# Optimization experiments

Hardware: AMD Instinct MI355X
Metric: run time of the kernel (lower is better)

## Reference

```python
import jax, jax.numpy as jnp
import numpy as np

MARGIN = 0.5  # init kwarg 'margin'
TWO_N, D = 8192, 256


def setup_inputs() -> dict:
    key = jax.random.key(0)
    k1, k2 = jax.random.split(key)
    embeddings = jax.random.normal(k1, (TWO_N, D), dtype=jnp.float32)
    neg_mask = jax.random.bernoulli(k2, 0.5, (TWO_N, TWO_N))  # bool [2N, 2N]
    return {"embeddings": embeddings, "neg_mask": neg_mask}


def _cdist(x, y):
    # Euclidean pairwise distances via the Gram trick (matches torch.cdist p=2)
    x2 = jnp.sum(x * x, axis=-1)[:, None]
    y2 = jnp.sum(y * y, axis=-1)[None, :]
    sq = jnp.maximum(x2 + y2 - 2.0 * (x @ y.T), 0.0)
    return jnp.sqrt(sq + 1e-12)


def reference(embeddings, neg_mask):
    two_n = embeddings.shape[0]
    n = two_n // 2
    d = _cdist(embeddings, embeddings)  # [2N, 2N]
    # masked sum of exp(margin - d) per anchor row (vectorizes the python loop)
    exp_neg = jnp.where(neg_mask, jnp.exp(MARGIN - d), 0.0)
    row_sums = exp_neg.sum(axis=1)  # [2N]
    idx = jnp.arange(n)
    ap = d[idx, idx + n]  # anchor-positive distances [N]
    j = jnp.log(row_sums[:n] + row_sums[n:]) + ap  # [N]
    # original skips NaN entries before the mean
    valid = ~jnp.isnan(j)
    r2 = jnp.where(valid, jnp.square(jnp.maximum(j, 0.0)), 0.0)
    cnt = jnp.maximum(valid.sum(), 1).astype(r2.dtype)
    loss = r2.sum() / cnt / 2.0
    return loss
```

## Files before the change

kernel.cpp:

```cpp
#include <hip/hip_runtime.h>
#include <hip/hip_bf16.h>
#include <stdint.h>

#define TWO_N  8192
#define NHALF  4096
#define DDIM   256
#define MARGIN 0.5f
#define NTRI   2080

static const size_t OFF_EMB  = 0;
static const size_t OFF_X2   = 4u * 1024 * 1024;
static const size_t OFF_AP   = OFF_X2 + (size_t)TWO_N * 4;
static const size_t OFF_FLAG = OFF_AP + (size_t)NHALF * 4;
static const size_t OFF_PART = OFF_FLAG + 256;
static const size_t OFF_RS   = OFF_PART + 64ull * TWO_N * 4;

typedef __attribute__((ext_vector_type(8))) short bf16x8;
typedef __attribute__((ext_vector_type(4))) float f32x4;

__device__ inline ushort f2bf(float f) {
  uint32_t u = __float_as_uint(f);
  uint32_t r = (u + 0x7FFFu + ((u >> 16) & 1u)) >> 16;
  return (ushort)r;
}
__device__ inline float bf2f(ushort h) { return __uint_as_float((uint32_t)h << 16); }

__device__ inline void gload_lds16(const void* g, void* l) {
  __builtin_amdgcn_global_load_lds(
      (const __attribute__((address_space(1))) uint32_t*)(uintptr_t)g,
      (__attribute__((address_space(3))) uint32_t*)(uint32_t)(uintptr_t)l,
      16, 0, 0);
}

#define STR2(x) #x
#define WAITVM(N) asm volatile("s_waitcnt vmcnt(" STR2(N) ")" ::: "memory")

__global__ __launch_bounds__(256) void smv2_prep(
    const float* __restrict__ emb,
    const uint32_t* __restrict__ maskw,
    ushort* __restrict__ emb_bf,
    float* __restrict__ x2,
    int* __restrict__ flag)
{
  const int t = threadIdx.x;
  if (blockIdx.x == 0) {
    __shared__ int sflag;
    if (t == 0) sflag = 0;
    __syncthreads();
    int found = 0;
    #pragma unroll
    for (int k = 0; k < 8; ++k) {
      uint32_t w = maskw[t * 8 + k];
      if (w > 1u && (w & 0xFEFEFEFEu) == 0u) found = 1;
    }
    if (found) atomicOr(&sflag, 1);
    __syncthreads();
    if (t == 0) *flag = sflag;
  }
  const int row  = blockIdx.x * 8 + (t >> 5);
  const int lane = t & 31;
  const float* rp = emb + (size_t)row * DDIM + lane * 8;
  float4 v0 = *(const float4*)(rp);
  float4 v1 = *(const float4*)(rp + 4);
  float vals[8] = {v0.x, v0.y, v0.z, v0.w, v1.x, v1.y, v1.z, v1.w};
  uint32_t packed[4];
  float ss = 0.f;
  #pragma unroll
  for (int k = 0; k < 4; ++k) {
    ushort h0 = f2bf(vals[2 * k]);
    ushort h1 = f2bf(vals[2 * k + 1]);
    packed[k] = (uint32_t)h0 | ((uint32_t)h1 << 16);
    float f0 = bf2f(h0), f1 = bf2f(h1);
    ss += f0 * f0 + f1 * f1;
  }
  *(uint4*)(emb_bf + (size_t)row * DDIM + lane * 8) =
      make_uint4(packed[0], packed[1], packed[2], packed[3]);
  #pragma unroll
  for (int m = 1; m < 32; m <<= 1) ss += __shfl_xor(ss, m);
  if (lane == 0) x2[row] = ss;
}

__global__ __launch_bounds__(512, 4) void smv2_main(
    const ushort* __restrict__ emb_bf,
    const float* __restrict__ x2,
    const uint8_t* __restrict__ mask8,
    const int* __restrict__ flagp,
    float* __restrict__ ap,
    float* __restrict__ partial)
{
  __shared__ char bufA[3 * 8192];
  __shared__ char bufB[3 * 8192];
  __shared__ uint8_t ldsM[128 * 128];
  __shared__ float ldsX[256];

  const int t = threadIdx.x;

  const int bid = blockIdx.x;
  const int idx = (bid & 7) * (NTRI / 8) + (bid >> 3);
  float rf = sqrtf(8.f * (float)idx + 1.f);
  int bx = (int)((rf - 1.f) * 0.5f);
  while ((bx + 1) * (bx + 2) / 2 <= idx) ++bx;
  while (bx * (bx + 1) / 2 > idx) --bx;
  const int by = idx - bx * (bx + 1) / 2;
  const int brow = by * 128;
  const int bcol = bx * 128;
  const bool diag = (bx == by);

  const char* gA = (const char*)(emb_bf + (size_t)brow * DDIM);
  const char* gB = (const char*)(emb_bf + (size_t)bcol * DDIM);

  const int srow = t >> 2;
  const int scb  = ((t & 3) * 16) ^ (((srow >> 1) & 3) << 4);
  const size_t gAoff = (size_t)srow * 512 + scb;
  const size_t gBoff = gAoff;
  const int ldst = t * 16;

  const int w  = t >> 6;
  const int l  = t & 63;
  const int wr = w >> 2;
  const int wc = w & 3;
  const int cl = l & 15;
  const int kh = l >> 4;

  int aoff[4], boff[2];
  #pragma unroll
  for (int m = 0; m < 4; ++m) {
    const int row = wr * 64 + m * 16 + cl;
    aoff[m] = row * 64 + ((kh * 16) ^ (((row >> 1) & 3) << 4));
  }
  #pragma unroll
  for (int n = 0; n < 2; ++n) {
    const int row = wc * 32 + n * 16 + cl;
    boff[n] = row * 64 + ((kh * 16) ^ (((row >> 1) & 3) << 4));
  }

  f32x4 acc[4][2];
  #pragma unroll
  for (int m = 0; m < 4; ++m)
    #pragma unroll
    for (int n = 0; n < 2; ++n) {
      f32x4 z = {0.f, 0.f, 0.f, 0.f};
      acc[m][n] = z;
    }
  uint32_t m2r[2][4];

#define STAGE(Q)                                                            \
  {                                                                         \
    gload_lds16(gA + gAoff + (Q) * 64, bufA + ((Q) % 3) * 8192 + ldst);     \
    gload_lds16(gB + gBoff + (Q) * 64, bufB + ((Q) % 3) * 8192 + ldst);     \
  }

#define M2LOAD                                                              \
  {                                                                         \
    _Pragma("unroll")                                                       \
    for (int n = 0; n < 2; ++n) {                                           \
      const int gj = bcol + wc * 32 + n * 16 + cl;                          \
      _Pragma("unroll")                                                     \
      for (int m = 0; m < 4; ++m)                                           \
        m2r[n][m] = *(const uint32_t*)(mask8 + (size_t)gj * TWO_N + brow +  \
                                       wr * 64 + m * 16 + kh * 4);          \
    }                                                                       \
  }

#define COMPUTE(P)                                                          \
  {                                                                         \
    const char* ba = bufA + ((P) % 3) * 8192;                               \
    const char* bb = bufB + ((P) % 3) * 8192;                               \
    bf16x8 a0 = *(const bf16x8*)(ba + aoff[0]);                             \
    bf16x8 a1 = *(const bf16x8*)(ba + aoff[1]);                             \
    bf16x8 a2 = *(const bf16x8*)(ba + aoff[2]);                             \
    bf16x8 a3 = *(const bf16x8*)(ba + aoff[3]);                             \
    bf16x8 b0 = *(const bf16x8*)(bb + boff[0]);                             \
    bf16x8 b1 = *(const bf16x8*)(bb + boff[1]);                             \
    acc[0][0] = __builtin_amdgcn_mfma_f32_16x16x32_bf16(a0, b0, acc[0][0], 0, 0, 0); \
    acc[0][1] = __builtin_amdgcn_mfma_f32_16x16x32_bf16(a0, b1, acc[0][1], 0, 0, 0); \
    acc[1][0] = __builtin_amdgcn_mfma_f32_16x16x32_bf16(a1, b0, acc[1][0], 0, 0, 0); \
    acc[1][1] = __builtin_amdgcn_mfma_f32_16x16x32_bf16(a1, b1, acc[1][1], 0, 0, 0); \
    acc[2][0] = __builtin_amdgcn_mfma_f32_16x16x32_bf16(a2, b0, acc[2][0], 0, 0, 0); \
    acc[2][1] = __builtin_amdgcn_mfma_f32_16x16x32_bf16(a2, b1, acc[2][1], 0, 0, 0); \
    acc[3][0] = __builtin_amdgcn_mfma_f32_16x16x32_bf16(a3, b0, acc[3][0], 0, 0, 0); \
    acc[3][1] = __builtin_amdgcn_mfma_f32_16x16x32_bf16(a3, b1, acc[3][1], 0, 0, 0); \
  }

#define PHASE(P, NW, SQ, DOM2)                                              \
  {                                                                         \
    WAITVM(NW);                                                             \
    __builtin_amdgcn_s_barrier();                                           \
    __builtin_amdgcn_sched_barrier(0);                                      \
    if ((SQ) >= 0) STAGE((SQ) < 0 ? 0 : (SQ));                              \
    if (DOM2) M2LOAD;                                                       \
    __builtin_amdgcn_sched_barrier(0);                                      \
    COMPUTE(P);                                                             \
  }

  STAGE(0);
  STAGE(1);
  #pragma unroll
  for (int it = 0; it < 2; ++it) {
    const int dl   = it * 8192 + t * 16;
    const int mrow = dl >> 7;
    const int mc   = dl & 127;
    const int msw  = ((mrow >> 2) & 3) << 5;
    gload_lds16(mask8 + (size_t)(brow + mrow) * TWO_N + bcol + (mc ^ msw), ldsM + dl);
  }
  {
    const float* src = (l < 32) ? (x2 + brow + l * 4) : (x2 + bcol + (l - 32) * 4);
    gload_lds16(src, (char*)ldsX + l * 16);
  }

  PHASE(0, 5, 2, 0)
  PHASE(1, 5, 3, 0)
  PHASE(2, 2, 4, 0)
  PHASE(3, 2, 5, 1)
  PHASE(4, 10, 6, 0)
  PHASE(5, 10, 7, 0)
  PHASE(6, 2, -1, 0)
  PHASE(7, 0, -1, 0)

  const int isByte = *flagp;
  const uint32_t* maskww = (const uint32_t*)mask8;

  float* part  = (float*)bufA;
  float* part2 = (float*)bufB;
  float cs[2] = {0.f, 0.f};

  #pragma unroll
  for (int m = 0; m < 4; ++m) {
    #pragma unroll
    for (int q = 0; q < 4; ++q) {
      const int lrow = wr * 64 + m * 16 + kh * 4 + q;
      const int gi = brow + lrow;
      const float xi = ldsX[lrow];
      const int msw = kh << 5;
      float rp = 0.f;
      #pragma unroll
      for (int n = 0; n < 2; ++n) {
        const int jc = wc * 32 + n * 16 + cl;
        const int gj = bcol + jc;
        const float g = acc[m][n][q];
        float sq = (gi == gj) ? 0.f : (xi + ldsX[128 + jc] - 2.f * g);
        sq = fmaxf(sq, 0.f) + 1e-12f;
        const float dd = __builtin_amdgcn_sqrtf(sq);
        if (gj == gi + NHALF && gi < NHALF) ap[gi] = dd;
        const float e = __expf(MARGIN - dd);
        bool mk1;
        if (isByte) mk1 = ldsM[lrow * 128 + (jc ^ msw)] != 0;
        else        mk1 = maskww[(size_t)gi * TWO_N + gj] != 0u;
        rp += mk1 ? e : 0.f;
        if (!diag) {
          bool mk2;
          if (isByte) mk2 = ((m2r[n][m] >> (8 * q)) & 255u) != 0u;
          else        mk2 = maskww[(size_t)gj * TWO_N + gi] != 0u;
          cs[n] += mk2 ? e : 0.f;
        }
      }
      #pragma unroll
      for (int s = 1; s < 16; s <<= 1) rp += __shfl_xor(rp, s);
      if (cl == 0) part[wc * 128 + lrow] = rp;
    }
  }

  if (!diag) {
    #pragma unroll
    for (int n = 0; n < 2; ++n) {
      cs[n] += __shfl_xor(cs[n], 16);
      cs[n] += __shfl_xor(cs[n], 32);
      if (l < 16) part2[wr * 128 + wc * 32 + n * 16 + l] = cs[n];
    }
  }
  __syncthreads();

  if (t < 128) {
    partial[(size_t)bx * TWO_N + brow + t] =
        (part[t] + part[128 + t]) + (part[256 + t] + part[384 + t]);
    if (!diag)
      partial[(size_t)by * TWO_N + bcol + t] = part2[t] + part2[128 + t];
  }
#undef PHASE
#undef COMPUTE
#undef M2LOAD
#undef STAGE
}

__global__ __launch_bounds__(256) void smv2_rowsum(
    const float* __restrict__ partial, float* __restrict__ rs)
{
  const int row = blockIdx.x * 256 + threadIdx.x;
  float s = 0.f;
  #pragma unroll 8
  for (int b = 0; b < 64; ++b) s += partial[(size_t)b * TWO_N + row];
  rs[row] = s;
}

__global__ __launch_bounds__(1024) void smv2_finalize(
    const float* __restrict__ rs, const float* __restrict__ ap,
    float* __restrict__ out)
{
  const int t = threadIdx.x;
  float sum = 0.f, cnt = 0.f;
  for (int i = t; i < NHALF; i += 1024) {
    float rsum = rs[i] + rs[i + NHALF];
    float jv = logf(rsum) + ap[i];
    if (!isnan(jv)) {
      cnt += 1.f;
      float mj = fmaxf(jv, 0.f);
      sum += mj * mj;
    }
  }
  __shared__ float ssum[16], scnt[16];
  #pragma unroll
  for (int s = 32; s >= 1; s >>= 1) {
    sum += __shfl_down(sum, s);
    cnt += __shfl_down(cnt, s);
  }
  const int wid = t >> 6, lid = t & 63;
  if (lid == 0) { ssum[wid] = sum; scnt[wid] = cnt; }
  __syncthreads();
  if (t == 0) {
    float S = 0.f, C = 0.f;
    #pragma unroll
    for (int i = 0; i < 16; ++i) { S += ssum[i]; C += scnt[i]; }
    if (C < 1.f) C = 1.f;
    out[0] = S / C * 0.5f;
  }
}

extern "C" void kernel_launch(void* const* d_in, const int* in_sizes, int n_in,
                              void* d_out, int out_size, void* d_ws, size_t ws_size,
                              hipStream_t stream) {
  const float* emb = (const float*)d_in[0];
  const void* mask = d_in[1];
  char* ws = (char*)d_ws;

  ushort* emb_bf = (ushort*)(ws + OFF_EMB);
  float*  x2     = (float*)(ws + OFF_X2);
  float*  ap     = (float*)(ws + OFF_AP);
  int*    flag   = (int*)(ws + OFF_FLAG);
  float*  part   = (float*)(ws + OFF_PART);
  float*  rs     = (float*)(ws + OFF_RS);

  smv2_prep<<<1024, 256, 0, stream>>>(emb, (const uint32_t*)mask, emb_bf, x2, flag);
  smv2_main<<<NTRI, 512, 0, stream>>>(emb_bf, x2, (const uint8_t*)mask, flag, ap, part);
  smv2_rowsum<<<32, 256, 0, stream>>>(part, rs);
  smv2_finalize<<<1, 1024, 0, stream>>>(rs, ap, (float*)d_out);
}
```

Baseline: 490.5 us.

## Pack mask into bitmap, simplify main pipeline, and accumulate row sums atomically

Adds a pack kernel that compresses the byte or word mask into a 1-bit-per-entry bitmap. The main kernel then reads small bitmap words for both the row and the transposed mask, instead of 16 KB byte tiles plus strided column loads. The main loop drops from triple to double buffering with plain barriers, and the occupancy hint rises to 8 blocks per CU. Per-tile partial row sums go to the result through atomics, which removes the separate row-sum kernel. In exchange it adds a full pass over the 64 MB mask, makes float accumulation order nondeterministic, and may leave the simpler pipeline less able to overlap loads with compute.

```diff
diff --git a/kernel.cpp b/kernel.cpp
--- a/kernel.cpp
+++ b/kernel.cpp
@@ -12,8 +12,8 @@
 static const size_t OFF_X2   = 4u * 1024 * 1024;
 static const size_t OFF_AP   = OFF_X2 + (size_t)TWO_N * 4;
 static const size_t OFF_FLAG = OFF_AP + (size_t)NHALF * 4;
-static const size_t OFF_PART = OFF_FLAG + 256;
-static const size_t OFF_RS   = OFF_PART + 64ull * TWO_N * 4;
+static const size_t OFF_BITM = 5u * 1024 * 1024;
+static const size_t OFF_RS   = 13u * 1024 * 1024;
 
 typedef __attribute__((ext_vector_type(8))) short bf16x8;
 typedef __attribute__((ext_vector_type(4))) float f32x4;
@@ -31,9 +31,12 @@
       (__attribute__((address_space(3))) uint32_t*)(uint32_t)(uintptr_t)l,
       16, 0, 0);
 }
-
-#define STR2(x) #x
-#define WAITVM(N) asm volatile("s_waitcnt vmcnt(" STR2(N) ")" ::: "memory")
+__device__ inline void gload_lds4(const void* g, void* l) {
+  __builtin_amdgcn_global_load_lds(
+      (const __attribute__((address_space(1))) uint32_t*)(uintptr_t)g,
+      (__attribute__((address_space(3))) uint32_t*)(uint32_t)(uintptr_t)l,
+      4, 0, 0);
+}
 
 __global__ __launch_bounds__(256) void smv2_prep(
     const float* __restrict__ emb,
@@ -80,17 +83,62 @@
   if (lane == 0) x2[row] = ss;
 }
 
-__global__ __launch_bounds__(512, 4) void smv2_main(
+__global__ __launch_bounds__(256) void smv2_pack(
+    const uint8_t* __restrict__ mask8,
+    const int* __restrict__ flagp,
+    uint32_t* __restrict__ bitM,
+    float* __restrict__ rs)
+{
+  const int t = threadIdx.x;
+  if (blockIdx.x == 0) {
+    float4 z = {0.f, 0.f, 0.f, 0.f};
+    #pragma unroll
+    for (int i = 0; i < 8; ++i) ((float4*)rs)[t * 8 + i] = z;
+  }
+  const int tid = blockIdx.x * 256 + t;
+  const int isByte = *flagp;
+  if (isByte) {
+    #pragma unroll
+    for (int it = 0; it < 4; ++it) {
+      const int idx = it * (2048 * 256) + tid;
+      const uint4 a = ((const uint4*)mask8)[(size_t)idx * 2];
+      const uint4 b = ((const uint4*)mask8)[(size_t)idx * 2 + 1];
+      const uint32_t wsv[8] = {a.x, a.y, a.z, a.w, b.x, b.y, b.z, b.w};
+      uint32_t out = 0;
+      #pragma unroll
+      for (int j = 0; j < 8; ++j)
+        out |= ((((wsv[j] & 0x01010101u) * 0x01020408u) >> 24) & 0xFu) << (4 * j);
+      bitM[idx] = out;
+    }
+  } else {
+    const uint32_t* maskw = (const uint32_t*)mask8;
+    #pragma unroll
+    for (int it = 0; it < 4; ++it) {
+      const int idx = it * (2048 * 256) + tid;
+      uint32_t out = 0;
+      #pragma unroll
+      for (int j = 0; j < 8; ++j) {
+        const uint4 wv = ((const uint4*)maskw)[(size_t)idx * 8 + j];
+        out |= (wv.x != 0u ? 1u : 0u) << (4 * j);
+        out |= (wv.y != 0u ? 1u : 0u) << (4 * j + 1);
+        out |= (wv.z != 0u ? 1u : 0u) << (4 * j + 2);
+        out |= (wv.w != 0u ? 1u : 0u) << (4 * j + 3);
+      }
+      bitM[idx] = out;
+    }
+  }
+}
+
+__global__ __launch_bounds__(512, 8) void smv2_main(
     const ushort* __restrict__ emb_bf,
     const float* __restrict__ x2,
-    const uint8_t* __restrict__ mask8,
-    const int* __restrict__ flagp,
+    const uint8_t* __restrict__ bitM,
     float* __restrict__ ap,
-    float* __restrict__ partial)
+    float* __restrict__ rs)
 {
-  __shared__ char bufA[3 * 8192];
-  __shared__ char bufB[3 * 8192];
-  __shared__ uint8_t ldsM[128 * 128];
+  __shared__ char bufA[2 * 8192];
+  __shared__ char bufB[2 * 8192];
+  __shared__ uint32_t ldsM[512];
   __shared__ float ldsX[256];
 
   const int t = threadIdx.x;
@@ -111,8 +159,7 @@
 
   const int srow = t >> 2;
   const int scb  = ((t & 3) * 16) ^ (((srow >> 1) & 3) << 4);
-  const size_t gAoff = (size_t)srow * 512 + scb;
-  const size_t gBoff = gAoff;
+  const size_t gOff = (size_t)srow * 512 + scb;
   const int ldst = t * 16;
 
   const int w  = t >> 6;
@@ -142,30 +189,36 @@
       f32x4 z = {0.f, 0.f, 0.f, 0.f};
       acc[m][n] = z;
     }
-  uint32_t m2r[2][4];
+
+  uint2 m2[2];
+  #pragma unroll
+  for (int n = 0; n < 2; ++n) {
+    const int gj = bcol + wc * 32 + n * 16 + cl;
+    m2[n] = *(const uint2*)(bitM + (size_t)gj * 1024 + (brow >> 3) + wr * 8);
+  }
+  __builtin_amdgcn_sched_barrier(0);
+
+  gload_lds4(bitM + (size_t)(brow + srow) * 1024 + (bcol >> 3) + (t & 3) * 4,
+             (char*)ldsM + t * 4);
+  {
+    const int xi = t & 255;
+    const float* src = (xi < 128) ? (x2 + brow + xi) : (x2 + bcol + (xi - 128));
+    gload_lds4(src, (char*)ldsX + xi * 4);
+  }
+  gload_lds16(gA + gOff, bufA + ldst);
+  gload_lds16(gB + gOff, bufB + ldst);
+  __syncthreads();
 
 #define STAGE(Q)                                                            \
   {                                                                         \
-    gload_lds16(gA + gAoff + (Q) * 64, bufA + ((Q) % 3) * 8192 + ldst);     \
-    gload_lds16(gB + gBoff + (Q) * 64, bufB + ((Q) % 3) * 8192 + ldst);     \
-  }
-
-#define M2LOAD                                                              \
-  {                                                                         \
-    _Pragma("unroll")                                                       \
-    for (int n = 0; n < 2; ++n) {                                           \
-      const int gj = bcol + wc * 32 + n * 16 + cl;                          \
-      _Pragma("unroll")                                                     \
-      for (int m = 0; m < 4; ++m)                                           \
-        m2r[n][m] = *(const uint32_t*)(mask8 + (size_t)gj * TWO_N + brow +  \
-                                       wr * 64 + m * 16 + kh * 4);          \
-    }                                                                       \
+    gload_lds16(gA + gOff + (Q) * 64, bufA + ((Q) & 1) * 8192 + ldst);      \
+    gload_lds16(gB + gOff + (Q) * 64, bufB + ((Q) & 1) * 8192 + ldst);      \
   }
 
 #define COMPUTE(P)                                                          \
   {                                                                         \
-    const char* ba = bufA + ((P) % 3) * 8192;                               \
-    const char* bb = bufB + ((P) % 3) * 8192;                               \
+    const char* ba = bufA + ((P) & 1) * 8192;                               \
+    const char* bb = bufB + ((P) & 1) * 8192;                               \
     bf16x8 a0 = *(const bf16x8*)(ba + aoff[0]);                             \
     bf16x8 a1 = *(const bf16x8*)(ba + aoff[1]);                             \
     bf16x8 a2 = *(const bf16x8*)(ba + aoff[2]);                             \
@@ -182,43 +235,15 @@
     acc[3][1] = __builtin_amdgcn_mfma_f32_16x16x32_bf16(a3, b1, acc[3][1], 0, 0, 0); \
   }
 
-#define PHASE(P, NW, SQ, DOM2)                                              \
+#define PHASE(P)                                                            \
   {                                                                         \
-    WAITVM(NW);                                                             \
-    __builtin_amdgcn_s_barrier();                                           \
-    __builtin_amdgcn_sched_barrier(0);                                      \
-    if ((SQ) >= 0) STAGE((SQ) < 0 ? 0 : (SQ));                              \
-    if (DOM2) M2LOAD;                                                       \
+    if ((P) < 7) STAGE((P) + 1);                                            \
     __builtin_amdgcn_sched_barrier(0);                                      \
     COMPUTE(P);                                                             \
-  }
-
-  STAGE(0);
-  STAGE(1);
-  #pragma unroll
-  for (int it = 0; it < 2; ++it) {
-    const int dl   = it * 8192 + t * 16;
-    const int mrow = dl >> 7;
-    const int mc   = dl & 127;
-    const int msw  = ((mrow >> 2) & 3) << 5;
-    gload_lds16(mask8 + (size_t)(brow + mrow) * TWO_N + bcol + (mc ^ msw), ldsM + dl);
-  }
-  {
-    const float* src = (l < 32) ? (x2 + brow + l * 4) : (x2 + bcol + (l - 32) * 4);
-    gload_lds16(src, (char*)ldsX + l * 16);
-  }
-
-  PHASE(0, 5, 2, 0)
-  PHASE(1, 5, 3, 0)
-  PHASE(2, 2, 4, 0)
-  PHASE(3, 2, 5, 1)
-  PHASE(4, 10, 6, 0)
-  PHASE(5, 10, 7, 0)
-  PHASE(6, 2, -1, 0)
-  PHASE(7, 0, -1, 0)
-
-  const int isByte = *flagp;
-  const uint32_t* maskww = (const uint32_t*)mask8;
+    __syncthreads();                                                        \
+  }
+
+  PHASE(0) PHASE(1) PHASE(2) PHASE(3) PHASE(4) PHASE(5) PHASE(6) PHASE(7)
 
   float* part  = (float*)bufA;
   float* part2 = (float*)bufB;
@@ -231,7 +256,7 @@
       const int lrow = wr * 64 + m * 16 + kh * 4 + q;
       const int gi = brow + lrow;
       const float xi = ldsX[lrow];
-      const int msw = kh << 5;
+      const uint32_t m1w = ldsM[lrow * 4 + wc];
       float rp = 0.f;
       #pragma unroll
       for (int n = 0; n < 2; ++n) {
@@ -243,16 +268,11 @@
         const float dd = __builtin_amdgcn_sqrtf(sq);
         if (gj == gi + NHALF && gi < NHALF) ap[gi] = dd;
         const float e = __expf(MARGIN - dd);
-        bool mk1;
-        if (isByte) mk1 = ldsM[lrow * 128 + (jc ^ msw)] != 0;
-        else        mk1 = maskww[(size_t)gi * TWO_N + gj] != 0u;
+        const uint32_t mk1 = (m1w >> (n * 16 + cl)) & 1u;
         rp += mk1 ? e : 0.f;
-        if (!diag) {
-          bool mk2;
-          if (isByte) mk2 = ((m2r[n][m] >> (8 * q)) & 255u) != 0u;
-          else        mk2 = maskww[(size_t)gj * TWO_N + gi] != 0u;
-          cs[n] += mk2 ? e : 0.f;
-        }
+        const uint32_t m2bits = (m < 2) ? m2[n].x : m2[n].y;
+        const uint32_t mk2 = (m2bits >> ((m & 1) * 16 + kh * 4 + q)) & 1u;
+        cs[n] += mk2 ? e : 0.f;
       }
       #pragma unroll
       for (int s = 1; s < 16; s <<= 1) rp += __shfl_xor(rp, s);
@@ -260,36 +280,23 @@
     }
   }
 
-  if (!diag) {
-    #pragma unroll
-    for (int n = 0; n < 2; ++n) {
-      cs[n] += __shfl_xor(cs[n], 16);
-      cs[n] += __shfl_xor(cs[n], 32);
-      if (l < 16) part2[wr * 128 + wc * 32 + n * 16 + l] = cs[n];
-    }
+  #pragma unroll
+  for (int n = 0; n < 2; ++n) {
+    cs[n] += __shfl_xor(cs[n], 16);
+    cs[n] += __shfl_xor(cs[n], 32);
+    if (l < 16) part2[wr * 128 + wc * 32 + n * 16 + l] = cs[n];
   }
   __syncthreads();
 
   if (t < 128) {
-    partial[(size_t)bx * TWO_N + brow + t] =
-        (part[t] + part[128 + t]) + (part[256 + t] + part[384 + t]);
+    atomicAdd(&rs[brow + t],
+              (part[t] + part[128 + t]) + (part[256 + t] + part[384 + t]));
     if (!diag)
-      partial[(size_t)by * TWO_N + bcol + t] = part2[t] + part2[128 + t];
+      atomicAdd(&rs[bcol + t], part2[t] + part2[128 + t]);
   }
 #undef PHASE
 #undef COMPUTE
-#undef M2LOAD
 #undef STAGE
-}
-
-__global__ __launch_bounds__(256) void smv2_rowsum(
-    const float* __restrict__ partial, float* __restrict__ rs)
-{
-  const int row = blockIdx.x * 256 + threadIdx.x;
-  float s = 0.f;
-  #pragma unroll 8
-  for (int b = 0; b < 64; ++b) s += partial[(size_t)b * TWO_N + row];
-  rs[row] = s;
 }
 
 __global__ __launch_bounds__(1024) void smv2_finalize(
@@ -332,15 +339,15 @@
   const void* mask = d_in[1];
   char* ws = (char*)d_ws;
 
-  ushort* emb_bf = (ushort*)(ws + OFF_EMB);
-  float*  x2     = (float*)(ws + OFF_X2);
-  float*  ap     = (float*)(ws + OFF_AP);
-  int*    flag   = (int*)(ws + OFF_FLAG);
-  float*  part   = (float*)(ws + OFF_PART);
-  float*  rs     = (float*)(ws + OFF_RS);
+  ushort*   emb_bf = (ushort*)(ws + OFF_EMB);
+  float*    x2     = (float*)(ws + OFF_X2);
+  float*    ap     = (float*)(ws + OFF_AP);
+  int*      flag   = (int*)(ws + OFF_FLAG);
+  uint32_t* bitM   = (uint32_t*)(ws + OFF_BITM);
+  float*    rs     = (float*)(ws + OFF_RS);
 
   smv2_prep<<<1024, 256, 0, stream>>>(emb, (const uint32_t*)mask, emb_bf, x2, flag);
-  smv2_main<<<NTRI, 512, 0, stream>>>(emb_bf, x2, (const uint8_t*)mask, flag, ap, part);
-  smv2_rowsum<<<32, 256, 0, stream>>>(part, rs);
+  smv2_pack<<<2048, 256, 0, stream>>>((const uint8_t*)mask, flag, bitM, rs);
+  smv2_main<<<NTRI, 512, 0, stream>>>(emb_bf, x2, (const uint8_t*)bitM, ap, rs);
   smv2_finalize<<<1, 1024, 0, stream>>>(rs, ap, (float*)d_out);
 }
```

Result: faster. 441.9 us (-9.9%).
